# Kernel tuning notes

Hardware: AMD Instinct MI355X
Metric: run time of the kernel (lower is better)

The kernel has to match this reference:

```python
import jax, jax.numpy as jnp
import numpy as np

B, C_IN, H, W = 32, 64, 64, 64
D, O, S_SP, K = 256, 512, 4, 3


def setup_inputs() -> dict:
    key = jax.random.key(0)
    k1, k2, k3, k4, k5 = jax.random.split(key, 5)
    x = jax.random.normal(k1, (B, C_IN, H, W), dtype=jnp.float32)
    dictionary = jax.random.normal(k2, (D, C_IN, K, K), dtype=jnp.float32)
    lookup_coefficients = jax.random.normal(k3, (O, S_SP), dtype=jnp.float32)
    bias = jax.random.normal(k4, (O,), dtype=jnp.float32)
    lookup_indices = jax.random.randint(k5, (O, S_SP), 0, D)
    return {
        "x": x,
        "dictionary": dictionary,
        "lookup_coefficients": lookup_coefficients,
        "bias": bias,
        "lookup_indices": lookup_indices,
    }


def reference(x, dictionary, lookup_coefficients, bias, lookup_indices):
    # Dictionary conv: S has shape [B, D, H, W] (stride 1, padding 1, 3x3 kernel)
    S = jax.lax.conv_general_dilated(
        x, dictionary,
        window_strides=(1, 1),
        padding=((1, 1), (1, 1)),
        dimension_numbers=("NCHW", "OIHW", "NCHW"),
    )
    # Build dense [O, D] combine matrix via scatter-add (duplicate indices
    # accumulate, matching the original += loop), then one GEMM.
    rows = jnp.arange(O)[:, None]  # [O, 1] broadcast against [O, sparsity]
    Wc = jnp.zeros((O, D), dtype=S.dtype).at[rows, lookup_indices].add(lookup_coefficients)
    out = jnp.einsum("bdhw,od->bohw", S, Wc)
    return out + bias[None, :, None, None]
```

## Files before the change

### kernel.cpp

```cpp
#include <hip/hip_runtime.h>
#include <stdint.h>

#define NB 32
#define NC 64
#define NH 64
#define NW 64
#define NO 512
#define HP 66

typedef __bf16 bf16x8 __attribute__((ext_vector_type(8)));
typedef short  s16x8  __attribute__((ext_vector_type(8)));
typedef float  f32x4  __attribute__((ext_vector_type(4)));

__device__ __forceinline__ uint16_t f2bf(float f) {
  uint32_t u = __builtin_bit_cast(uint32_t, f);
  u += 0x7fffu + ((u >> 16) & 1u);
  return (uint16_t)(u >> 16);
}

__device__ __forceinline__ void gld16(const uint16_t* g, uint16_t* l) {
  __builtin_amdgcn_global_load_lds(
      (const __attribute__((address_space(1))) void*)(g),
      (__attribute__((address_space(3))) void*)(l), 16, 0, 0);
}

__global__ void k_build_w(const float* __restrict__ dict,
                          const float* __restrict__ coef,
                          const int*   __restrict__ idx,
                          uint16_t*    __restrict__ Wl) {
  __shared__ float tmp[576];
  const int o = blockIdx.x;
  const int t = threadIdx.x;
  float v = 0.f;
#pragma unroll
  for (int s = 0; s < 4; ++s)
    v += coef[o * 4 + s] * dict[idx[o * 4 + s] * 576 + t];
  tmp[t] = v;
  __syncthreads();
  const int c = t & 63, p = t >> 6;
  const int sl = ((p * NO + o) * 8 + ((c >> 3) ^ (o & 7))) * 8 + (c & 7);
  Wl[sl] = f2bf(tmp[c * 9 + p]);
}

__global__ void k_nhwc(const float* __restrict__ x, uint16_t* __restrict__ xh) {
  const int bh = blockIdx.x;
  const int b = bh / HP, hp = bh % HP;
  const int t = threadIdx.x;
  uint16_t* row = xh + (size_t)(b * HP + hp) * 4096;
  if (hp == 0 || hp == HP - 1) {
    int4* r4 = reinterpret_cast<int4*>(row);
    r4[t]       = int4{0, 0, 0, 0};
    r4[t + 256] = int4{0, 0, 0, 0};
    return;
  }
  __shared__ float tile[64][65];
  const int h = hp - 1;
  const int w = t & 63;
#pragma unroll
  for (int c = (t >> 6); c < 64; c += 4)
    tile[c][w] = x[((size_t)(b * NC + c) * NH + h) * NW + w];
  __syncthreads();
#pragma unroll
  for (int i = 0; i < 2; ++i) {
    const int s = t + i * 256;
    const int w2 = s >> 3, cb = s & 7;
    uint32_t d[4];
#pragma unroll
    for (int j = 0; j < 4; ++j) {
      const uint32_t lo = f2bf(tile[cb * 8 + 2 * j][w2]);
      const uint32_t hi = f2bf(tile[cb * 8 + 2 * j + 1][w2]);
      d[j] = lo | (hi << 16);
    }
    reinterpret_cast<int4*>(row)[w2 * 8 + (cb ^ (w2 & 7))] =
        int4{(int)d[0], (int)d[1], (int)d[2], (int)d[3]};
  }
}

__global__ __launch_bounds__(512, 2) void k_conv(
    const uint16_t* __restrict__ xh,
    const uint16_t* __restrict__ Wl,
    const float*    __restrict__ bias,
    float*          __restrict__ out) {
  __shared__ __align__(16) uint16_t xs[10 * 66 * 64];
  __shared__ __align__(16) uint16_t as[3 * 128 * 64];

  const int t = threadIdx.x;
  const int flat = blockIdx.x;
  const int s    = (flat & 7) * 128 + (flat >> 3);
  const int ot   = s & 3;
  const int gy   = s >> 2;
  const int o0 = ot * 128;
  const int b  = gy >> 3;
  const int h0 = (gy & 7) * 8;

  const int lane = t & 63;
  const int wid  = t >> 6;

  if (t < 160) {
    const int r = t >> 4, sl = (t >> 3) & 1, j = t & 7;
    reinterpret_cast<int4*>(xs)[r * 528 + sl * 520 + j] = int4{0, 0, 0, 0};
  }

  {
    const uint16_t* srow = xh + (size_t)(b * HP + h0 + wid) * 4096;
    uint16_t* drow = xs + wid * 4224 + 64;
#pragma unroll
    for (int k = 0; k < 8; ++k)
      gld16(srow + k * 512 + lane * 8, drow + k * 512);
    const int r2 = 8 + (wid >> 2);
    const int kb = (wid & 3) * 2;
    const uint16_t* srow2 = xh + (size_t)(b * HP + h0 + r2) * 4096;
    uint16_t* drow2 = xs + r2 * 4224 + 64;
    gld16(srow2 + kb * 512 + lane * 8, drow2 + kb * 512);
    gld16(srow2 + (kb + 1) * 512 + lane * 8, drow2 + (kb + 1) * 512);
  }

  auto stage_a = [&](int g) {
#pragma unroll
    for (int j = 0; j < 6; ++j) {
      const int c = wid * 6 + j;
      const int tap = c >> 4, k = c & 15;
      const uint16_t* src =
          Wl + (size_t)(tap * 3 + g) * 32768 + o0 * 64 + k * 512;
      gld16(src + lane * 8, as + tap * 8192 + k * 512);
    }
  };
  stage_a(0);

  const int wm  = wid & 1;
  const int wn  = wid >> 1;
  const int l15 = lane & 15;
  const int lg  = lane >> 4;

  f32x4 acc[4][8] = {};

  __syncthreads();

#pragma unroll
  for (int g = 0; g < 3; ++g) {
    const int dw = g - 1;

#pragma unroll
    for (int q = 0; q < 2; ++q) {
      bf16x8 braw[4][4];
#pragma unroll
      for (int rr = 0; rr < 4; ++rr) {
        const int rbase = (wn * 2 + rr) * 4224;
#pragma unroll
        for (int nw = 0; nw < 4; ++nw) {
          const int wv = nw * 16 + l15 + dw;
          const int cb = (q * 4 + lg) ^ (wv & 7);
          braw[rr][nw] = __builtin_bit_cast(bf16x8,
              *reinterpret_cast<const s16x8*>(xs + rbase + (wv + 1) * 64 + cb * 8));
        }
      }
#pragma unroll
      for (int dh = 0; dh < 3; ++dh) {
        bf16x8 af[4];
#pragma unroll
        for (int m = 0; m < 4; ++m) {
          const int orow = wm * 64 + m * 16 + l15;
          const int cb = (q * 4 + lg) ^ (orow & 7);
          af[m] = __builtin_bit_cast(bf16x8,
              *reinterpret_cast<const s16x8*>(as + dh * 8192 + orow * 64 + cb * 8));
        }
#pragma unroll
        for (int m = 0; m < 4; ++m)
#pragma unroll
          for (int n = 0; n < 8; ++n)
            acc[m][n] = __builtin_amdgcn_mfma_f32_16x16x32_bf16(
                af[m], braw[(n >> 2) + dh][n & 3], acc[m][n], 0, 0, 0);
      }
    }

    if (g < 2) {
      __syncthreads();
      stage_a(g + 1);
      __syncthreads();
    }
  }

  const int hb = h0 + wn * 2;
#pragma unroll
  for (int m = 0; m < 4; ++m) {
#pragma unroll
    for (int rr = 0; rr < 4; ++rr) {
      const int o = o0 + wm * 64 + m * 16 + lg * 4 + rr;
      const float bv = bias[o];
      float* op = out + ((size_t)(b * NO + o) * NH + hb) * NW;
#pragma unroll
      for (int n = 0; n < 8; ++n)
        op[(n >> 2) * NW + (n & 3) * 16 + l15] = acc[m][n][rr] + bv;
    }
  }
}

extern "C" void kernel_launch(void* const* d_in, const int* in_sizes, int n_in,
                              void* d_out, int out_size, void* d_ws, size_t ws_size,
                              hipStream_t stream) {
  const float* x    = (const float*)d_in[0];
  const float* dict = (const float*)d_in[1];
  const float* coef = (const float*)d_in[2];
  const float* bias = (const float*)d_in[3];
  const int*   idx  = (const int*)d_in[4];
  float* out = (float*)d_out;

  uint16_t* xh = (uint16_t*)d_ws;
  uint16_t* Wl = (uint16_t*)((char*)d_ws + (18u << 20));

  hipLaunchKernelGGL(k_build_w, dim3(NO), dim3(576), 0, stream, dict, coef, idx, Wl);
  hipLaunchKernelGGL(k_nhwc, dim3(NB * HP), dim3(256), 0, stream, x, xh);
  hipLaunchKernelGGL(k_conv, dim3(1024), dim3(512), 0, stream, xh, Wl, bias, out);
}
```

Baseline: 113.0 us.

## Stage conv output through LDS for vectorized nontemporal stores; simplify B-fragment addressing

The epilogue now writes each warp's accumulator tile into LDS (reusing the input tile buffer after a barrier), then reads it back as float4 rows and issues 16-byte nontemporal global stores with the bias added. This replaces scattered 4-byte stores and is meant to cut store instruction count and improve write coalescing on the 67 MB output. The B-operand LDS address is also hoisted, using the fact that nw*16 leaves the swizzle bits unchanged. The cost is an extra barrier plus an LDS round trip per m-slice.

```diff
diff --git a/kernel.cpp b/kernel.cpp
--- a/kernel.cpp
+++ b/kernel.cpp
@@ -142,17 +142,16 @@
 
 #pragma unroll
     for (int q = 0; q < 2; ++q) {
+      const int cbB = (q * 4 + lg) ^ ((l15 + dw) & 7);
       bf16x8 braw[4][4];
 #pragma unroll
       for (int rr = 0; rr < 4; ++rr) {
-        const int rbase = (wn * 2 + rr) * 4224;
-#pragma unroll
-        for (int nw = 0; nw < 4; ++nw) {
-          const int wv = nw * 16 + l15 + dw;
-          const int cb = (q * 4 + lg) ^ (wv & 7);
+        const uint16_t* rb =
+            xs + (wn * 2 + rr) * 4224 + (l15 + dw + 1) * 64 + cbB * 8;
+#pragma unroll
+        for (int nw = 0; nw < 4; ++nw)
           braw[rr][nw] = __builtin_bit_cast(bf16x8,
-              *reinterpret_cast<const s16x8*>(xs + rbase + (wv + 1) * 64 + cb * 8));
-        }
+              *reinterpret_cast<const s16x8*>(rb + nw * 1024));
       }
 #pragma unroll
       for (int dh = 0; dh < 3; ++dh) {
@@ -180,17 +179,30 @@
     }
   }
 
+  __syncthreads();
+  float* tb = reinterpret_cast<float*>(xs) + wid * 2048;
   const int hb = h0 + wn * 2;
 #pragma unroll
   for (int m = 0; m < 4; ++m) {
 #pragma unroll
-    for (int rr = 0; rr < 4; ++rr) {
-      const int o = o0 + wm * 64 + m * 16 + lg * 4 + rr;
+    for (int n = 0; n < 8; ++n) {
+      const int pix = (n >> 2) * 64 + (n & 3) * 16 + l15;
+#pragma unroll
+      for (int rr = 0; rr < 4; ++rr)
+        tb[(lg * 4 + rr) * 128 + pix] = acc[m][n][rr];
+    }
+#pragma unroll
+    for (int j = 0; j < 8; ++j) {
+      const int r  = j * 64 + lane;
+      const int op = r >> 5;
+      const int px = (r & 31) * 4;
+      f32x4 v = reinterpret_cast<f32x4*>(tb)[r];
+      const int o = o0 + wm * 64 + m * 16 + op;
       const float bv = bias[o];
-      float* op = out + ((size_t)(b * NO + o) * NH + hb) * NW;
-#pragma unroll
-      for (int n = 0; n < 8; ++n)
-        op[(n >> 2) * NW + (n & 3) * 16 + l15] = acc[m][n][rr] + bv;
+      v[0] += bv; v[1] += bv; v[2] += bv; v[3] += bv;
+      float* dst = out +
+          ((size_t)(b * NO + o) * NH + hb + (px >> 6)) * NW + (px & 63);
+      __builtin_nontemporal_store(v, reinterpret_cast<f32x4*>(dst));
     }
   }
 }
```

Result: slower. 115.7 us (+2.4%).

## Switch conv to 32x32 MFMA, pre-pad NHWC rows, fuse prep kernels

Applied to the files above, without the earlier changes.

Merges the weight-build and NHWC conversion kernels into one launch. The NHWC buffer now carries the width padding, so the conv kernel can load its input tile as one contiguous block without zero-filling shared memory. The main loop moves from 16x16x32 to 32x32x16 bf16 MFMA, with each wave owning one output row across all 128 channels. Stores become 16-byte nontemporal vector writes and bias is loaded before the main loop. These changes aim to cut launch overhead, LDS reads per MFMA and store transactions, but they change register pressure and the LDS access pattern.

```diff
diff --git a/kernel.cpp b/kernel.cpp
--- a/kernel.cpp
+++ b/kernel.cpp
@@ -6,11 +6,11 @@
 #define NH 64
 #define NW 64
 #define NO 512
-#define HP 66
 
 typedef __bf16 bf16x8 __attribute__((ext_vector_type(8)));
 typedef short  s16x8  __attribute__((ext_vector_type(8)));
 typedef float  f32x4  __attribute__((ext_vector_type(4)));
+typedef float  f32x16 __attribute__((ext_vector_type(16)));
 
 __device__ __forceinline__ uint16_t f2bf(float f) {
   uint32_t u = __builtin_bit_cast(uint32_t, f);
@@ -24,33 +24,46 @@
       (__attribute__((address_space(3))) void*)(l), 16, 0, 0);
 }
 
-__global__ void k_build_w(const float* __restrict__ dict,
-                          const float* __restrict__ coef,
-                          const int*   __restrict__ idx,
-                          uint16_t*    __restrict__ Wl) {
-  __shared__ float tmp[576];
-  const int o = blockIdx.x;
+__global__ void k_prep(const float* __restrict__ dict,
+                       const float* __restrict__ coef,
+                       const int*   __restrict__ idx,
+                       const float* __restrict__ x,
+                       uint16_t*    __restrict__ Wl,
+                       uint16_t*    __restrict__ xh) {
+  const int bid = blockIdx.x;
   const int t = threadIdx.x;
-  float v = 0.f;
-#pragma unroll
-  for (int s = 0; s < 4; ++s)
-    v += coef[o * 4 + s] * dict[idx[o * 4 + s] * 576 + t];
-  tmp[t] = v;
-  __syncthreads();
-  const int c = t & 63, p = t >> 6;
-  const int sl = ((p * NO + o) * 8 + ((c >> 3) ^ (o & 7))) * 8 + (c & 7);
-  Wl[sl] = f2bf(tmp[c * 9 + p]);
-}
-
-__global__ void k_nhwc(const float* __restrict__ x, uint16_t* __restrict__ xh) {
-  const int bh = blockIdx.x;
-  const int b = bh / HP, hp = bh % HP;
-  const int t = threadIdx.x;
-  uint16_t* row = xh + (size_t)(b * HP + hp) * 4096;
-  if (hp == 0 || hp == HP - 1) {
-    int4* r4 = reinterpret_cast<int4*>(row);
-    r4[t]       = int4{0, 0, 0, 0};
-    r4[t + 256] = int4{0, 0, 0, 0};
+  if (bid < NO) {
+    __shared__ float tmp[576];
+    const int o = bid;
+#pragma unroll
+    for (int j = 0; j < 3; ++j) {
+      const int id = t + j * 256;
+      if (id < 576) {
+        float v = 0.f;
+#pragma unroll
+        for (int s = 0; s < 4; ++s)
+          v += coef[o * 4 + s] * dict[idx[o * 4 + s] * 576 + id];
+        tmp[id] = v;
+      }
+    }
+    __syncthreads();
+#pragma unroll
+    for (int j = 0; j < 3; ++j) {
+      const int id = t + j * 256;
+      if (id < 576) {
+        const int c = id & 63, p = id >> 6;
+        const int sl = ((p * NO + o) * 8 + ((c >> 3) ^ (o & 7))) * 8 + (c & 7);
+        Wl[sl] = f2bf(tmp[c * 9 + p]);
+      }
+    }
+    return;
+  }
+  const int bh = bid - NO;
+  const int b = bh / 66, hp = bh % 66;
+  uint16_t* row = xh + (size_t)(b * 66 + hp) * 4224;
+  int4* r4 = reinterpret_cast<int4*>(row);
+  if (hp == 0 || hp == 65) {
+    for (int j = t; j < 528; j += 256) r4[j] = int4{0, 0, 0, 0};
     return;
   }
   __shared__ float tile[64][65];
@@ -60,10 +73,13 @@
   for (int c = (t >> 6); c < 64; c += 4)
     tile[c][w] = x[((size_t)(b * NC + c) * NH + h) * NW + w];
   __syncthreads();
+  if (t < 16)
+    r4[(t >> 3) * 520 + (t & 7)] = int4{0, 0, 0, 0};
 #pragma unroll
   for (int i = 0; i < 2; ++i) {
     const int s = t + i * 256;
     const int w2 = s >> 3, cb = s & 7;
+    const int wp = w2 + 1;
     uint32_t d[4];
 #pragma unroll
     for (int j = 0; j < 4; ++j) {
@@ -71,7 +87,7 @@
       const uint32_t hi = f2bf(tile[cb * 8 + 2 * j + 1][w2]);
       d[j] = lo | (hi << 16);
     }
-    reinterpret_cast<int4*>(row)[w2 * 8 + (cb ^ (w2 & 7))] =
+    r4[wp * 8 + (cb ^ (wp & 7))] =
         int4{(int)d[0], (int)d[1], (int)d[2], (int)d[3]};
   }
 }
@@ -81,38 +97,33 @@
     const uint16_t* __restrict__ Wl,
     const float*    __restrict__ bias,
     float*          __restrict__ out) {
-  __shared__ __align__(16) uint16_t xs[10 * 66 * 64];
+  __shared__ __align__(16) uint16_t xs[10 * 4224];
   __shared__ __align__(16) uint16_t as[3 * 128 * 64];
 
   const int t = threadIdx.x;
+  const int lane = t & 63;
+  const int wid  = t >> 6;
   const int flat = blockIdx.x;
   const int s    = (flat & 7) * 128 + (flat >> 3);
   const int ot   = s & 3;
-  const int gy   = s >> 2;
-  const int o0 = ot * 128;
-  const int b  = gy >> 3;
-  const int h0 = (gy & 7) * 8;
-
-  const int lane = t & 63;
-  const int wid  = t >> 6;
-
-  if (t < 160) {
-    const int r = t >> 4, sl = (t >> 3) & 1, j = t & 7;
-    reinterpret_cast<int4*>(xs)[r * 528 + sl * 520 + j] = int4{0, 0, 0, 0};
-  }
+  const int pt   = s >> 2;
+  const int O0 = ot * 128;
+  const int b  = pt >> 3;
+  const int h0 = (pt & 7) * 8;
 
   {
-    const uint16_t* srow = xh + (size_t)(b * HP + h0 + wid) * 4096;
-    uint16_t* drow = xs + wid * 4224 + 64;
-#pragma unroll
-    for (int k = 0; k < 8; ++k)
-      gld16(srow + k * 512 + lane * 8, drow + k * 512);
-    const int r2 = 8 + (wid >> 2);
-    const int kb = (wid & 3) * 2;
-    const uint16_t* srow2 = xh + (size_t)(b * HP + h0 + r2) * 4096;
-    uint16_t* drow2 = xs + r2 * 4224 + 64;
-    gld16(srow2 + kb * 512 + lane * 8, drow2 + kb * 512);
-    gld16(srow2 + (kb + 1) * 512 + lane * 8, drow2 + (kb + 1) * 512);
+    const uint16_t* src = xh + (size_t)(b * 66 + h0) * 4224;
+#pragma unroll
+    for (int j = 0; j < 10; ++j) {
+      const int ch = wid + j * 8;
+      gld16(src + ch * 512 + lane * 8, xs + ch * 512);
+    }
+    if (wid < 2) {
+      const int ch = 80 + wid;
+      gld16(src + ch * 512 + lane * 8, xs + ch * 512);
+    }
+    if (wid == 2 && lane < 32)
+      gld16(src + 41984 + lane * 8, xs + 41984 + lane * 8);
   }
 
   auto stage_a = [&](int g) {
@@ -121,58 +132,57 @@
       const int c = wid * 6 + j;
       const int tap = c >> 4, k = c & 15;
       const uint16_t* src =
-          Wl + (size_t)(tap * 3 + g) * 32768 + o0 * 64 + k * 512;
+          Wl + (size_t)(tap * 3 + g) * 32768 + (O0 + k * 8) * 64;
       gld16(src + lane * 8, as + tap * 8192 + k * 512);
     }
   };
   stage_a(0);
 
-  const int wm  = wid & 1;
-  const int wn  = wid >> 1;
-  const int l15 = lane & 15;
-  const int lg  = lane >> 4;
-
-  f32x4 acc[4][8] = {};
+  const int wn  = wid;
+  const int l31 = lane & 31;
+  const int hi  = lane >> 5;
+
+  float bvv[4];
+#pragma unroll
+  for (int ob = 0; ob < 4; ++ob)
+    bvv[ob] = bias[O0 + ob * 32 + l31];
+
+  f32x16 acc[2][4] = {};
 
   __syncthreads();
 
 #pragma unroll
   for (int g = 0; g < 3; ++g) {
     const int dw = g - 1;
-
-#pragma unroll
-    for (int q = 0; q < 2; ++q) {
-      bf16x8 braw[4][4];
-#pragma unroll
-      for (int rr = 0; rr < 4; ++rr) {
-        const int rbase = (wn * 2 + rr) * 4224;
-#pragma unroll
-        for (int nw = 0; nw < 4; ++nw) {
-          const int wv = nw * 16 + l15 + dw;
-          const int cb = (q * 4 + lg) ^ (wv & 7);
-          braw[rr][nw] = __builtin_bit_cast(bf16x8,
-              *reinterpret_cast<const s16x8*>(xs + rbase + (wv + 1) * 64 + cb * 8));
+#pragma unroll
+    for (int dh = 0; dh < 3; ++dh) {
+      const uint16_t* xrow = xs + (wn + dh) * 4224;
+#pragma unroll
+      for (int q = 0; q < 4; ++q) {
+        bf16x8 braw[2], af[4];
+#pragma unroll
+        for (int pb = 0; pb < 2; ++pb) {
+          const int wp = pb * 32 + l31 + dw + 1;
+          const int slot = (q * 2 + hi) ^ (wp & 7);
+          braw[pb] = __builtin_bit_cast(bf16x8,
+              *reinterpret_cast<const s16x8*>(xrow + wp * 64 + slot * 8));
         }
-      }
-#pragma unroll
-      for (int dh = 0; dh < 3; ++dh) {
-        bf16x8 af[4];
-#pragma unroll
-        for (int m = 0; m < 4; ++m) {
-          const int orow = wm * 64 + m * 16 + l15;
-          const int cb = (q * 4 + lg) ^ (orow & 7);
-          af[m] = __builtin_bit_cast(bf16x8,
-              *reinterpret_cast<const s16x8*>(as + dh * 8192 + orow * 64 + cb * 8));
+#pragma unroll
+        for (int ob = 0; ob < 4; ++ob) {
+          const int orow = ob * 32 + l31;
+          const int slot = (q * 2 + hi) ^ (orow & 7);
+          af[ob] = __builtin_bit_cast(bf16x8,
+              *reinterpret_cast<const s16x8*>(
+                  as + dh * 8192 + orow * 64 + slot * 8));
         }
 #pragma unroll
-        for (int m = 0; m < 4; ++m)
-#pragma unroll
-          for (int n = 0; n < 8; ++n)
-            acc[m][n] = __builtin_amdgcn_mfma_f32_16x16x32_bf16(
-                af[m], braw[(n >> 2) + dh][n & 3], acc[m][n], 0, 0, 0);
-      }
-    }
-
+        for (int pb = 0; pb < 2; ++pb)
+#pragma unroll
+          for (int ob = 0; ob < 4; ++ob)
+            acc[pb][ob] = __builtin_amdgcn_mfma_f32_32x32x16_bf16(
+                braw[pb], af[ob], acc[pb][ob], 0, 0, 0);
+      }
+    }
     if (g < 2) {
       __syncthreads();
       stage_a(g + 1);
@@ -180,17 +190,24 @@
     }
   }
 
-  const int hb = h0 + wn * 2;
-#pragma unroll
-  for (int m = 0; m < 4; ++m) {
-#pragma unroll
-    for (int rr = 0; rr < 4; ++rr) {
-      const int o = o0 + wm * 64 + m * 16 + lg * 4 + rr;
-      const float bv = bias[o];
-      float* op = out + ((size_t)(b * NO + o) * NH + hb) * NW;
-#pragma unroll
-      for (int n = 0; n < 8; ++n)
-        op[(n >> 2) * NW + (n & 3) * 16 + l15] = acc[m][n][rr] + bv;
+  const int h = h0 + wn;
+#pragma unroll
+  for (int pb = 0; pb < 2; ++pb) {
+#pragma unroll
+    for (int ob = 0; ob < 4; ++ob) {
+      const int o = O0 + ob * 32 + l31;
+      const float bv = bvv[ob];
+      float* obase = out + ((size_t)(b * NO + o) * NH + h) * NW;
+#pragma unroll
+      for (int r4 = 0; r4 < 4; ++r4) {
+        f32x4 v;
+        v[0] = acc[pb][ob][r4 * 4 + 0] + bv;
+        v[1] = acc[pb][ob][r4 * 4 + 1] + bv;
+        v[2] = acc[pb][ob][r4 * 4 + 2] + bv;
+        v[3] = acc[pb][ob][r4 * 4 + 3] + bv;
+        const int w = pb * 32 + r4 * 8 + hi * 4;
+        __builtin_nontemporal_store(v, reinterpret_cast<f32x4*>(obase + w));
+      }
     }
   }
 }
@@ -208,7 +225,8 @@
   uint16_t* xh = (uint16_t*)d_ws;
   uint16_t* Wl = (uint16_t*)((char*)d_ws + (18u << 20));
 
-  hipLaunchKernelGGL(k_build_w, dim3(NO), dim3(576), 0, stream, dict, coef, idx, Wl);
-  hipLaunchKernelGGL(k_nhwc, dim3(NB * HP), dim3(256), 0, stream, x, xh);
-  hipLaunchKernelGGL(k_conv, dim3(1024), dim3(512), 0, stream, xh, Wl, bias, out);
-}
+  hipLaunchKernelGGL(k_prep, dim3(NO + NB * 66), dim3(256), 0, stream,
+                     dict, coef, idx, x, Wl, xh);
+  hipLaunchKernelGGL(k_conv, dim3(1024), dim3(512), 0, stream,
+                     xh, Wl, bias, out);
+}
```

Measured after the change: 277.2 us. 2.45x slower.
